# Kernel tuning notes

Hardware: AMD Instinct MI355X
Metric: run time of the kernel (lower is better)

## Reference

```python
import jax, jax.numpy as jnp
import numpy as np

BS, T, D_IN, NH, D_OUT = 8, 1024, 64, 8, 1024
DK = 2


def setup_inputs() -> dict:
    key = jax.random.key(0)
    ks = jax.random.split(key, 10)
    X = jax.random.normal(ks[0], (BS, T, D_IN), dtype=jnp.float32)
    # Linear(d_in, 2*Nh) params (torch stores weight as (out, in))
    Wq_w = jax.random.normal(ks[1], (2 * NH, D_IN), dtype=jnp.float32) * (1.0 / np.sqrt(D_IN))
    Wq_b = jax.random.normal(ks[2], (2 * NH,), dtype=jnp.float32) * 0.02
    Wk_w = jax.random.normal(ks[3], (2 * NH, D_IN), dtype=jnp.float32) * (1.0 / np.sqrt(D_IN))
    Wk_b = jax.random.normal(ks[4], (2 * NH,), dtype=jnp.float32) * 0.02
    Wkey_ = jax.random.normal(ks[5], (2, 2), dtype=jnp.float32)
    u = jax.random.normal(ks[6], (T, 2), dtype=jnp.float32)
    # R[t,l] = [(l-t)^2, (l-t)]
    rel = jnp.arange(T)[None, :] - jnp.arange(T)[:, None]  # (T,T)
    R = jnp.stack([rel.astype(jnp.float32) ** 2, rel.astype(jnp.float32)], axis=-1)  # (T,T,2)
    attention_center = jax.random.normal(ks[7], (NH, 1), dtype=jnp.float32) * 2.0
    alpha = jax.random.normal(ks[8], (1,), dtype=jnp.float32)
    W_w = jax.random.normal(ks[9], (D_OUT, T), dtype=jnp.float32) * (1.0 / np.sqrt(T))
    W_b = jnp.zeros((D_OUT,), dtype=jnp.float32)
    return {"X": X, "Wq_w": Wq_w, "Wq_b": Wq_b, "Wk_w": Wk_w, "Wk_b": Wk_b,
            "Wkey_": Wkey_, "u": u, "R": R, "attention_center": attention_center,
            "alpha": alpha, "W_w": W_w, "W_b": W_b}


def reference(X, Wq_w, Wq_b, Wk_w, Wk_b, Wkey_, u, R, attention_center, alpha, W_w, W_b):
    bs, T_, d_in = X.shape
    Nh = attention_center.shape[0]
    query = (X @ Wq_w.T + Wq_b).reshape(bs, T_, Nh, DK)
    key_ = (X @ Wk_w.T + Wk_b).reshape(bs, T_, Nh, DK)
    r_delta = jnp.einsum('de,tle->tld', Wkey_, R)  # (T,T,2)
    v = -alpha * jnp.concatenate([jnp.ones_like(attention_center), -2.0 * attention_center], axis=-1)  # (Nh,2)
    first = jnp.einsum('bthd,blhd->bthl', query, key_)
    second = jnp.einsum('bthd,tld->bthl', query, r_delta)
    third = jnp.einsum('ld,bthd->blht', u, key_)  # added positionally, matching torch
    fourth = jnp.einsum('hd,tld->thl', v, r_delta)
    scores = first + second + third + fourth[None]  # (bs,T,Nh,T)
    probs = jax.nn.softmax(scores, axis=-1)
    iv = jnp.einsum('bthl,bld->bthd', probs, X)  # (bs,T,Nh,d_in)
    iv = iv.reshape(bs, T_, Nh * d_in).transpose(0, 2, 1)  # (bs, Nh*d_in, T)
    out = iv @ W_w.T + W_b  # (bs, Nh*d_in, d_out)
    return out
```

## Files before the change

kernel.cpp:

```cpp
#include <hip/hip_runtime.h>
#include <hip/hip_bf16.h>

#define BS   8
#define TT   1024
#define DIN  64
#define NH   8
#define DOUT 1024

typedef __attribute__((ext_vector_type(8))) short bf16x8;
typedef __attribute__((ext_vector_type(8))) unsigned short u16x8;
typedef __attribute__((ext_vector_type(4))) float f32x4;

typedef __attribute__((address_space(3))) unsigned int lds_u32;
typedef const __attribute__((address_space(1))) unsigned int glb_u32;

__device__ __forceinline__ unsigned short f2bf(float f) {
    unsigned int u = __float_as_uint(f);
    u += 0x7fff + ((u >> 16) & 1);
    return (unsigned short)(u >> 16);
}

__global__ __launch_bounds__(256) void prep_fused(const float* __restrict__ X,
                                                  const float* __restrict__ Wq_w,
                                                  const float* __restrict__ Wq_b,
                                                  const float* __restrict__ Wk_w,
                                                  const float* __restrict__ Wk_b,
                                                  const float* __restrict__ W_w,
                                                  float* __restrict__ Q,
                                                  float* __restrict__ K,
                                                  unsigned short* __restrict__ XtP,
                                                  unsigned short* __restrict__ Wbf) {
    __shared__ float Ws[32][65];
    __shared__ float bsm[32];
    __shared__ float Xs[8][64];
    __shared__ unsigned short S[64][68];

    const int bid = blockIdx.x, tid = threadIdx.x;

    if (bid < 1024) {
        for (int i = tid; i < 2048; i += 256) {
            int r = i >> 6, d = i & 63;
            Ws[r][d] = (r < 16) ? Wq_w[r * 64 + d] : Wk_w[(r - 16) * 64 + d];
        }
        if (tid < 32) bsm[tid] = (tid < 16) ? Wq_b[tid] : Wk_b[tid - 16];
        int row0 = bid * 8;
        for (int i = tid; i < 512; i += 256) {
            int r = i >> 6, d = i & 63;
            Xs[r][d] = X[(size_t)(row0 + r) * 64 + d];
        }
        __syncthreads();
        int r = tid >> 5;
        int j = tid & 31;
        float s = bsm[j];
        #pragma unroll
        for (int d = 0; d < 64; ++d) s = fmaf(Xs[r][d], Ws[j][d], s);
        int row = row0 + r;
        if (j < 16) {
            Q[(size_t)row * 16 + j] = s;
        } else {
            int h = (j - 16) >> 1, d2 = (j - 16) & 1;
            int b = row >> 10, l = row & 1023;
            K[(((size_t)(b * 8 + h)) * 1024 + l) * 2 + d2] = s;
        }
    } else if (bid < 1152) {
        int idx = bid - 1024;
        int bb = idx >> 4, lc = idx & 15;
        int l0 = lc * 64;
        int r = tid >> 4;
        int q4 = (tid & 15) * 4;
        #pragma unroll
        for (int p = 0; p < 4; ++p) {
            int row = p * 16 + r;
            float4 v = *(const float4*)(X + ((size_t)(bb * 1024 + l0 + row)) * 64 + q4);
            S[row][q4 + 0] = f2bf(v.x);
            S[row][q4 + 1] = f2bf(v.y);
            S[row][q4 + 2] = f2bf(v.z);
            S[row][q4 + 3] = f2bf(v.w);
        }
        __syncthreads();
        #pragma unroll
        for (int it = 0; it < 2; ++it) {
            int chunk = it * 256 + tid;
            int lane = chunk & 63, mi = (chunk >> 6) & 3, lbr = chunk >> 8;
            int g = lane >> 4, tr = lane & 15;
            int d = mi * 16 + tr;
            int ls = lbr * 32 + g * 8;
            u16x8 o;
            #pragma unroll
            for (int j = 0; j < 8; ++j) o[j] = S[ls + j][d];
            *(u16x8*)(XtP + (size_t)((((bb * 32 + lc * 2 + lbr) * 4 + mi) * 64 + lane)) * 8) = o;
        }
    } else {
        int i = (bid - 1152) * 256 + tid;
        float4 v = ((const float4*)W_w)[i];
        ushort4 o;
        o.x = f2bf(v.x); o.y = f2bf(v.y); o.z = f2bf(v.z); o.w = f2bf(v.w);
        ((ushort4*)Wbf)[i] = o;
    }
}

__global__ __launch_bounds__(512, 8) void attn_mfma(const unsigned short* __restrict__ XtP,
                                                    const float* __restrict__ Q,
                                                    const float* __restrict__ K,
                                                    const float* __restrict__ u,
                                                    const float* __restrict__ Wkey,
                                                    const float* __restrict__ center,
                                                    const float* __restrict__ alpha,
                                                    unsigned short* __restrict__ IV) {
    const int h  = blockIdx.y;
    const int bb = blockIdx.z;
    const int tid = threadIdx.x;
    const int w = tid >> 6, lane = tid & 63;
    const int g = lane >> 4, tr = lane & 15;
    const int tsub = w & 3, lhalf = w >> 2;
    const int t = blockIdx.x * 64 + tsub * 16 + tr;

    __shared__ float SH[4352];
    __shared__ unsigned short Xs[2][4096];
    __shared__ float red[8][4];

    const unsigned short* xsrc = XtP + (size_t)bb * 65536
                               + (size_t)((tid >> 8) * 16) * 2048 + (tid & 255) * 8;

    {
        const float4* Kg = (const float4*)(K + ((size_t)(bb * 8 + h)) * 2048);
        ((float4*)SH)[tid] = Kg[tid];
        __builtin_amdgcn_global_load_lds((glb_u32*)xsrc, (lds_u32*)(&Xs[0][tid * 8]), 16, 0, 0);
    }
    asm volatile("s_waitcnt vmcnt(0)");
    __syncthreads();

    float mxp, mxn, myp, myn;
    {
        const float2* K2 = (const float2*)SH;
        float2 ka = K2[tid], kb = K2[tid + 512];
        mxp = fmaxf(ka.x, kb.x); mxn = fminf(ka.x, kb.x);
        myp = fmaxf(ka.y, kb.y); myn = fminf(ka.y, kb.y);
        #pragma unroll
        for (int off = 32; off; off >>= 1) {
            mxp = fmaxf(mxp, __shfl_xor(mxp, off)); mxn = fminf(mxn, __shfl_xor(mxn, off));
            myp = fmaxf(myp, __shfl_xor(myp, off)); myn = fminf(myn, __shfl_xor(myn, off));
        }
        if (lane == 0) { red[w][0] = mxp; red[w][1] = mxn; red[w][2] = myp; red[w][3] = myn; }
    }
    __syncthreads();
    mxp = red[0][0]; mxn = red[0][1]; myp = red[0][2]; myn = red[0][3];
    #pragma unroll
    for (int i = 1; i < 8; ++i) {
        mxp = fmaxf(mxp, red[i][0]); mxn = fminf(mxn, red[i][1]);
        myp = fmaxf(myp, red[i][2]); myn = fminf(myn, red[i][3]);
    }

    const float L2E = 1.4426950408889634f;
    float2 q  = ((const float2*)Q)[(size_t)(bb * 1024 + t) * 8 + h];
    float2 uu = ((const float2*)u)[t];
    const float al = alpha[0];
    const float a0 = (q.x + uu.x) * L2E;
    const float a1 = (q.y + uu.y) * L2E;
    const float p0 = q.x - al;
    const float p1 = q.y + 2.0f * al * center[h];
    const float c0 = (p0 * Wkey[0] + p1 * Wkey[2]) * L2E;
    const float c1 = (p0 * Wkey[1] + p1 * Wkey[3]) * L2E;
    const float tf = (float)t;

    const float qb = fmaxf(a0 * mxp, a0 * mxn) + fmaxf(a1 * myp, a1 * myn);
    const float dlo = -tf, dhi = 1023.0f - tf;
    float qm = fmaxf(fmaf(fmaf(c0, dlo, c1), dlo, 0.0f),
                     fmaf(fmaf(c0, dhi, c1), dhi, 0.0f));
    if (c0 < 0.0f) {
        float dstar = -c1 / (2.0f * c0);
        if (dstar > dlo && dstar < dhi) qm = -c1 * c1 / (4.0f * c0);
    }
    const float negm = -(qm + qb);

    f32x4 acc[4];
    #pragma unroll
    for (int mi = 0; mi < 4; ++mi) acc[mi] = (f32x4){0.f, 0.f, 0.f, 0.f};
    float sum = 0.f;

    int cur = 0;
    for (int it = 0; it < 16; ++it) {
        const int itn = (it + 1) & 15;
        __builtin_amdgcn_global_load_lds((glb_u32*)(xsrc + itn * 2048),
                                         (lds_u32*)(&Xs[cur ^ 1][tid * 8]), 16, 0, 0);

        const int lb = lhalf * 512 + it * 32 + g * 8;
        const float4* kp = (const float4*)SH + (lb >> 1);
        const float dlb = (float)lb - tf;
        union { bf16x8 v; unsigned int wd[4]; } pb;
        #pragma unroll
        for (int jj = 0; jj < 4; ++jj) {
            float4 kv = kp[jj];
            float dl0 = dlb + (float)(2 * jj);
            float dl1 = dl0 + 1.0f;
            float e0 = exp2f(fmaf(fmaf(c0, dl0, c1), dl0, fmaf(a0, kv.x, fmaf(a1, kv.y, negm))));
            float e1 = exp2f(fmaf(fmaf(c0, dl1, c1), dl1, fmaf(a0, kv.z, fmaf(a1, kv.w, negm))));
            sum += e0 + e1;
            asm("v_cvt_pk_bf16_f32 %0, %1, %2" : "=v"(pb.wd[jj]) : "v"(e0), "v"(e1));
        }
        const bf16x8* xv = (const bf16x8*)(&Xs[cur][0]);
        #pragma unroll
        for (int mi = 0; mi < 4; ++mi)
            acc[mi] = __builtin_amdgcn_mfma_f32_16x16x32_bf16(
                xv[lhalf * 256 + mi * 64 + lane], pb.v, acc[mi], 0, 0, 0);

        asm volatile("s_waitcnt vmcnt(0)");
        __syncthreads();
        cur ^= 1;
    }

    sum += __shfl_xor(sum, 16);
    sum += __shfl_xor(sum, 32);

    __syncthreads();
    if (lhalf == 1) {
        float* cp = SH + (tsub * 64 + lane) * 17;
        #pragma unroll
        for (int mi = 0; mi < 4; ++mi)
            #pragma unroll
            for (int r = 0; r < 4; ++r) cp[mi * 4 + r] = acc[mi][r];
        cp[16] = sum;
    }
    __syncthreads();
    if (lhalf == 0) {
        const float* cp = SH + (tsub * 64 + lane) * 17;
        #pragma unroll
        for (int mi = 0; mi < 4; ++mi)
            #pragma unroll
            for (int r = 0; r < 4; ++r) acc[mi][r] += cp[mi * 4 + r];
        sum += cp[16];
        const float rinv = 1.0f / sum;
        #pragma unroll
        for (int mi = 0; mi < 4; ++mi) {
            #pragma unroll
            for (int r = 0; r < 4; ++r) {
                int d = mi * 16 + g * 4 + r;
                IV[((size_t)(bb * 512 + h * 64 + d)) * 1024 + t] = f2bf(acc[mi][r] * rinv);
            }
        }
    }
}

__global__ __launch_bounds__(512) void gemm_out(const unsigned short* __restrict__ IV,
                                                const unsigned short* __restrict__ Wbf,
                                                const float* __restrict__ W_b,
                                                float* __restrict__ out) {
    const int jt = blockIdx.x;
    const int mt = blockIdx.y;
    const int tid = threadIdx.x;
    const int w = tid >> 6, lane = tid & 63;
    const int lr = lane & 15, kg = lane >> 4;
    const int wr = w >> 2, wc = w & 3;

    __shared__ unsigned short As[4][8192];
    __shared__ unsigned short Bs[4][8192];

    const int r0 = tid >> 2, s0 = tid & 3;
    const int kga = s0 ^ ((r0 >> 1) & 3);
    const unsigned short* Ag = IV  + (size_t)(mt * 128 + r0) * 1024 + kga * 8;
    const unsigned short* Bg = Wbf + (size_t)(jt * 128 + r0) * 1024 + kga * 8;

#define STAGE(bufi, kk) do {                                                                           \
    __builtin_amdgcn_global_load_lds((glb_u32*)(Ag + (kk)), (lds_u32*)(&As[bufi][tid * 8]), 16, 0, 0); \
    __builtin_amdgcn_global_load_lds((glb_u32*)(Bg + (kk)), (lds_u32*)(&Bs[bufi][tid * 8]), 16, 0, 0); \
} while (0)

    f32x4 acc[4][2];
    #pragma unroll
    for (int mi = 0; mi < 4; ++mi)
        #pragma unroll
        for (int ni = 0; ni < 2; ++ni)
            acc[mi][ni] = (f32x4){0.f, 0.f, 0.f, 0.f};

    STAGE(0, 0);
    STAGE(1, 32);
    STAGE(2, 64);

    const int slot = kg ^ ((lr >> 1) & 3);

    #pragma unroll
    for (int kt = 0; kt < 32; ++kt) {
        if (kt < 30)       asm volatile("s_waitcnt vmcnt(4)" ::: "memory");
        else if (kt == 30) asm volatile("s_waitcnt vmcnt(2)" ::: "memory");
        else               asm volatile("s_waitcnt vmcnt(0)" ::: "memory");
        __builtin_amdgcn_s_barrier();
        __builtin_amdgcn_sched_barrier(0);
        if (kt < 29) STAGE((kt + 3) & 3, (kt + 3) * 32);

        const int cur = kt & 3;
        bf16x8 af[4], bfr[2];
        #pragma unroll
        for (int mi = 0; mi < 4; ++mi) {
            int row = wr * 64 + mi * 16 + lr;
            af[mi] = *(const bf16x8*)(&As[cur][row * 32 + slot * 8]);
        }
        #pragma unroll
        for (int ni = 0; ni < 2; ++ni) {
            int row = wc * 32 + ni * 16 + lr;
            bfr[ni] = *(const bf16x8*)(&Bs[cur][row * 32 + slot * 8]);
        }
        #pragma unroll
        for (int mi = 0; mi < 4; ++mi)
            #pragma unroll
            for (int ni = 0; ni < 2; ++ni)
                acc[mi][ni] = __builtin_amdgcn_mfma_f32_16x16x32_bf16(
                    af[mi], bfr[ni], acc[mi][ni], 0, 0, 0);
    }
#undef STAGE

    float wb[2];
    #pragma unroll
    for (int ni = 0; ni < 2; ++ni) wb[ni] = W_b[jt * 128 + wc * 32 + ni * 16 + lr];

    #pragma unroll
    for (int mi = 0; mi < 4; ++mi) {
        #pragma unroll
        for (int ni = 0; ni < 2; ++ni) {
            #pragma unroll
            for (int r = 0; r < 4; ++r) {
                int m = mt * 128 + wr * 64 + mi * 16 + kg * 4 + r;
                int j = jt * 128 + wc * 32 + ni * 16 + lr;
                out[(size_t)m * 1024 + j] = acc[mi][ni][r] + wb[ni];
            }
        }
    }
}

extern "C" void kernel_launch(void* const* d_in, const int* in_sizes, int n_in,
                              void* d_out, int out_size, void* d_ws, size_t ws_size,
                              hipStream_t stream) {
    const float* X      = (const float*)d_in[0];
    const float* Wq_w   = (const float*)d_in[1];
    const float* Wq_b   = (const float*)d_in[2];
    const float* Wk_w   = (const float*)d_in[3];
    const float* Wk_b   = (const float*)d_in[4];
    const float* Wkey   = (const float*)d_in[5];
    const float* u      = (const float*)d_in[6];
    const float* center = (const float*)d_in[8];
    const float* alpha  = (const float*)d_in[9];
    const float* W_w    = (const float*)d_in[10];
    const float* W_b    = (const float*)d_in[11];
    float* out = (float*)d_out;

    char* ws = (char*)d_ws;
    unsigned short* XtP  = (unsigned short*)ws;
    float*          Qbuf = (float*)(ws + (1024u << 10));
    float*          Kbuf = (float*)(ws + (1536u << 10));
    unsigned short* Wbf  = (unsigned short*)(ws + (2048u << 10));
    unsigned short* IV   = (unsigned short*)(ws + (4096u << 10));

    prep_fused<<<2176, 256, 0, stream>>>(X, Wq_w, Wq_b, Wk_w, Wk_b, W_w, Qbuf, Kbuf, XtP, Wbf);
    attn_mfma<<<dim3(16, 8, 8), 512, 0, stream>>>(XtP, Qbuf, Kbuf, u, Wkey, center, alpha, IV);
    gemm_out<<<dim3(8, 32), 512, 0, stream>>>(IV, Wbf, W_b, out);
}
```

Before: 140.0 us.

## Triple-buffer X tiles in attention kernel with one barrier per iteration

Replaces the double-buffered X staging, which waited for all loads and synced at the end of each iteration, with a three-buffer ring. Loads run two iterations ahead and each step uses a partial vmcnt wait followed by a single barrier. The loop is fully unrolled, and the cross-half reduction scratch now reuses the X buffers. This aims to hide global-to-LDS latency and cut stalls, at the cost of more LDS (3x8KB plus 8KB for K), which may reduce occupancy.

```diff
diff --git a/kernel.cpp b/kernel.cpp
--- a/kernel.cpp
+++ b/kernel.cpp
@@ -115,24 +115,23 @@
     const int tsub = w & 3, lhalf = w >> 2;
     const int t = blockIdx.x * 64 + tsub * 16 + tr;
 
-    __shared__ float SH[4352];
-    __shared__ unsigned short Xs[2][4096];
+    __shared__ float Ks[2048];
+    __shared__ unsigned short Xs[3][4096];
     __shared__ float red[8][4];
+    float* Cc = (float*)&Xs[0][0];
 
     const unsigned short* xsrc = XtP + (size_t)bb * 65536
                                + (size_t)((tid >> 8) * 16) * 2048 + (tid & 255) * 8;
 
     {
         const float4* Kg = (const float4*)(K + ((size_t)(bb * 8 + h)) * 2048);
-        ((float4*)SH)[tid] = Kg[tid];
-        __builtin_amdgcn_global_load_lds((glb_u32*)xsrc, (lds_u32*)(&Xs[0][tid * 8]), 16, 0, 0);
-    }
-    asm volatile("s_waitcnt vmcnt(0)");
+        ((float4*)Ks)[tid] = Kg[tid];
+    }
     __syncthreads();
 
     float mxp, mxn, myp, myn;
     {
-        const float2* K2 = (const float2*)SH;
+        const float2* K2 = (const float2*)Ks;
         float2 ka = K2[tid], kb = K2[tid + 512];
         mxp = fmaxf(ka.x, kb.x); mxn = fminf(ka.x, kb.x);
         myp = fmaxf(ka.y, kb.y); myn = fminf(ka.y, kb.y);
@@ -178,14 +177,24 @@
     for (int mi = 0; mi < 4; ++mi) acc[mi] = (f32x4){0.f, 0.f, 0.f, 0.f};
     float sum = 0.f;
 
-    int cur = 0;
+#define XSTAGE(bufi, itx) \
+    __builtin_amdgcn_global_load_lds((glb_u32*)(xsrc + (itx) * 2048), \
+                                     (lds_u32*)(&Xs[bufi][tid * 8]), 16, 0, 0)
+
+    XSTAGE(0, 0);
+    XSTAGE(1, 1);
+
+    #pragma unroll
     for (int it = 0; it < 16; ++it) {
-        const int itn = (it + 1) & 15;
-        __builtin_amdgcn_global_load_lds((glb_u32*)(xsrc + itn * 2048),
-                                         (lds_u32*)(&Xs[cur ^ 1][tid * 8]), 16, 0, 0);
-
+        if (it < 15) asm volatile("s_waitcnt vmcnt(1)" ::: "memory");
+        else         asm volatile("s_waitcnt vmcnt(0)" ::: "memory");
+        __builtin_amdgcn_s_barrier();
+        __builtin_amdgcn_sched_barrier(0);
+        if (it < 14) XSTAGE((it + 2) % 3, it + 2);
+
+        const int cur = it % 3;
         const int lb = lhalf * 512 + it * 32 + g * 8;
-        const float4* kp = (const float4*)SH + (lb >> 1);
+        const float4* kp = (const float4*)Ks + (lb >> 1);
         const float dlb = (float)lb - tf;
         union { bf16x8 v; unsigned int wd[4]; } pb;
         #pragma unroll
@@ -203,18 +212,15 @@
         for (int mi = 0; mi < 4; ++mi)
             acc[mi] = __builtin_amdgcn_mfma_f32_16x16x32_bf16(
                 xv[lhalf * 256 + mi * 64 + lane], pb.v, acc[mi], 0, 0, 0);
-
-        asm volatile("s_waitcnt vmcnt(0)");
-        __syncthreads();
-        cur ^= 1;
-    }
+    }
+#undef XSTAGE
 
     sum += __shfl_xor(sum, 16);
     sum += __shfl_xor(sum, 32);
 
     __syncthreads();
     if (lhalf == 1) {
-        float* cp = SH + (tsub * 64 + lane) * 17;
+        float* cp = Cc + (tsub * 64 + lane) * 17;
         #pragma unroll
         for (int mi = 0; mi < 4; ++mi)
             #pragma unroll
@@ -223,7 +229,7 @@
     }
     __syncthreads();
     if (lhalf == 0) {
-        const float* cp = SH + (tsub * 64 + lane) * 17;
+        const float* cp = Cc + (tsub * 64 + lane) * 17;
         #pragma unroll
         for (int mi = 0; mi < 4; ++mi)
             #pragma unroll
```

Result: faster. 136.2 us (-2.7%).
